# Optimization experiments

Measured on AMD Instinct MI355X. Metric: run time of the kernel, lower is better.

Reference implementation:

```python
import jax, jax.numpy as jnp
import numpy as np

# ---- static configuration (matches init_kwargs) ----
B = 32
H = 56
W = 56
C = 192
HEADS = 6
WS = 7            # window size
SHIFT = 3         # shift size (WS // 2)
MLP_HIDDEN = 768  # 4 * C
CPB = 256         # clip(56*56//16, 256, 1024)
N = WS * WS       # tokens per window
NW = (H // WS) * (W // WS)  # windows per image
EPS = 1e-5

# ---- static tables (Swin V2 continuous relative position bias) ----
# log-spaced relative coords table: [(2*WS-1)^2, 2]
_r = np.arange(-(WS - 1), WS, dtype=np.float32)
_tab = np.stack(np.meshgrid(_r, _r, indexing='ij'), axis=-1)  # [2WS-1, 2WS-1, 2]
_tab = _tab / (WS - 1) * 8.0  # pretrained_window_size=0 -> use window_size-1
_tab = np.sign(_tab) * np.log2(np.abs(_tab) + 1.0) / np.log2(8.0)
REL_TABLE = jnp.asarray(_tab.reshape(-1, 2))

# relative position index: [N, N] into the (2WS-1)^2 table
_coords = np.stack(np.meshgrid(np.arange(WS), np.arange(WS), indexing='ij'))
_cf = _coords.reshape(2, -1)
_rel = (_cf[:, :, None] - _cf[:, None, :]).transpose(1, 2, 0).astype(np.int64)
_rel[..., 0] += WS - 1
_rel[..., 1] += WS - 1
_rel[..., 0] *= 2 * WS - 1
REL_INDEX = jnp.asarray(_rel.sum(-1))

# shifted-window attention mask: [NW, N, N] with 0 / -100
_img = np.zeros((H, W), dtype=np.float32)
_sl = [slice(0, -WS), slice(-WS, -SHIFT), slice(-SHIFT, None)]
_cnt = 0
for _hs in _sl:
    for _ws in _sl:
        _img[_hs, _ws] = _cnt
        _cnt += 1
_mw = _img.reshape(H // WS, WS, W // WS, WS).transpose(0, 2, 1, 3).reshape(-1, N)
_am = _mw[:, None, :] - _mw[:, :, None]
ATTN_MASK = jnp.asarray(np.where(_am != 0, -100.0, 0.0).astype(np.float32))


def _layer_norm(x, g, b):
    mu = jnp.mean(x, axis=-1, keepdims=True)
    var = jnp.mean(jnp.square(x - mu), axis=-1, keepdims=True)
    return (x - mu) * jax.lax.rsqrt(var + EPS) * g + b


def setup_inputs() -> dict:
    key = jax.random.key(0)
    ks = jax.random.split(key, 10)
    def n(k, shape, s=0.02):
        return jax.random.normal(k, shape, jnp.float32) * s
    return {
        'x': jax.random.normal(ks[0], (B, H * W, C), jnp.float32),
        'qkv_w': n(ks[1], (3 * C, C)),
        'q_bias': jnp.zeros((C,), jnp.float32),
        'v_bias': jnp.zeros((C,), jnp.float32),
        'logit_scale': jnp.full((HEADS, 1, 1), jnp.log(10.0), jnp.float32),
        'cpb_w1': n(ks[2], (CPB, 2)),
        'cpb_b1': jnp.zeros((CPB,), jnp.float32),
        'cpb_w2': n(ks[3], (HEADS, CPB)),
        'proj_w': n(ks[4], (C, C)),
        'proj_b': jnp.zeros((C,), jnp.float32),
        'norm1_g': jnp.ones((C,), jnp.float32),
        'norm1_b': jnp.zeros((C,), jnp.float32),
        'norm2_g': jnp.ones((C,), jnp.float32),
        'norm2_b': jnp.zeros((C,), jnp.float32),
        'fc1_w': n(ks[5], (MLP_HIDDEN, C)),
        'fc1_b': jnp.zeros((MLP_HIDDEN,), jnp.float32),
        'fc2_w': n(ks[6], (C, MLP_HIDDEN)),
        'fc2_b': jnp.zeros((C,), jnp.float32),
    }


def reference(x, qkv_w, q_bias, v_bias, logit_scale, cpb_w1, cpb_b1, cpb_w2,
              proj_w, proj_b, norm1_g, norm1_b, norm2_g, norm2_b,
              fc1_w, fc1_b, fc2_w, fc2_b):
    b = x.shape[0]
    hd = C // HEADS
    shortcut = x

    # cyclic shift + window partition -> [b*NW, N, C]
    xi = jnp.roll(x.reshape(b, H, W, C), (-SHIFT, -SHIFT), axis=(1, 2))
    xw = xi.reshape(b, H // WS, WS, W // WS, WS, C)
    xw = xw.transpose(0, 1, 3, 2, 4, 5).reshape(-1, N, C)

    # qkv projection (k has no bias, per Swin V2)
    qkv_bias = jnp.concatenate([q_bias, jnp.zeros_like(q_bias), v_bias])
    qkv = (xw @ qkv_w.T + qkv_bias).reshape(-1, N, 3, HEADS, hd)
    qkv = qkv.transpose(2, 0, 3, 1, 4)  # [3, bw, heads, N, hd]
    q, k, v = qkv[0], qkv[1], qkv[2]

    # cosine attention with learned logit scale
    q = q / jnp.maximum(jnp.linalg.norm(q, axis=-1, keepdims=True), 1e-12)
    k = k / jnp.maximum(jnp.linalg.norm(k, axis=-1, keepdims=True), 1e-12)
    scale = jnp.exp(jnp.minimum(logit_scale, jnp.log(100.0)))  # [heads,1,1]
    attn = jnp.einsum('bhnd,bhmd->bhnm', q, k) * scale

    # continuous relative position bias via tiny MLP
    tab = jax.nn.relu(REL_TABLE @ cpb_w1.T + cpb_b1) @ cpb_w2.T  # [(2WS-1)^2, heads]
    rpb = 16.0 * jax.nn.sigmoid(tab[REL_INDEX])                  # [N, N, heads]
    attn = attn + rpb.transpose(2, 0, 1)[None]

    # shifted-window mask + softmax
    attn = attn.reshape(-1, NW, HEADS, N, N) + ATTN_MASK[None, :, None]
    attn = jax.nn.softmax(attn.reshape(-1, HEADS, N, N), axis=-1)

    out = jnp.einsum('bhnm,bhmd->bhnd', attn, v)
    out = out.transpose(0, 2, 1, 3).reshape(-1, N, C) @ proj_w.T + proj_b

    # window reverse + reverse shift
    xr = out.reshape(b, H // WS, W // WS, WS, WS, C)
    xr = xr.transpose(0, 1, 3, 2, 4, 5).reshape(b, H, W, C)
    xr = jnp.roll(xr, (SHIFT, SHIFT), axis=(1, 2)).reshape(b, H * W, C)

    # post-norm residual (Swin V2 style)
    x1 = shortcut + _layer_norm(xr, norm1_g, norm1_b)
    hmid = jax.nn.silu(x1 @ fc1_w.T + fc1_b) @ fc2_w.T + fc2_b
    return x1 + _layer_norm(hmid, norm2_g, norm2_b)
```

## Files before the change

kernel.cpp:

```cpp
#include <hip/hip_runtime.h>


typedef unsigned short ushort_t;
using f32x4  = __attribute__((ext_vector_type(4))) float;
using short8 = __attribute__((ext_vector_type(8))) short;
union LD16 { short8 v; ushort4 h[2]; };

__device__ __forceinline__ ushort_t f2bf(float f) {
  union { float f; unsigned u; } v; v.f = f;
  unsigned r = v.u + 0x7fffu + ((v.u >> 16) & 1u);
  return (ushort_t)(r >> 16);
}
__device__ __forceinline__ float bf2f(ushort_t u) {
  union { unsigned u; float f; } v; v.u = ((unsigned)u) << 16;
  return v.f;
}

__device__ __forceinline__ int img_pos(int m) {
  int win = m / 49, n = m - win * 49;
  int b = win >> 6, wi = win & 63;
  int nd = n / 7, nm = n - nd * 7;
  int hs = (wi >> 3) * 7 + nd;
  int ws = (wi & 7) * 7 + nm;
  int h = hs + 3; if (h >= 56) h -= 56;
  int w = ws + 3; if (w >= 56) w -= 56;
  return b * 3136 + h * 56 + w;
}

__device__ __forceinline__ int region3(int a) { return a < 49 ? 0 : (a < 53 ? 1 : 2); }

__global__ void cvt_kernel(const float* __restrict__ in, ushort_t* __restrict__ out, int n) {
  int i = blockIdx.x * 256 + threadIdx.x;
  if (i < n) out[i] = f2bf(in[i]);
}

__global__ __launch_bounds__(256) void gather_cvt_kernel(
    const float* __restrict__ x, ushort_t* __restrict__ xw) {
  int i8 = blockIdx.x * 256 + threadIdx.x;
  int m = i8 / 24, c8 = (i8 - m * 24) * 8;
  const float* p = x + (size_t)img_pos(m) * 192 + c8;
  float4 a = *(const float4*)p, b = *(const float4*)(p + 4);
  ushort_t* q = xw + (size_t)m * 192 + c8;
  *(ushort4*)q       = make_ushort4(f2bf(a.x), f2bf(a.y), f2bf(a.z), f2bf(a.w));
  *(ushort4*)(q + 4) = make_ushort4(f2bf(b.x), f2bf(b.y), f2bf(b.z), f2bf(b.w));
}

__global__ __launch_bounds__(256) void cpb_kernel(
    const float* __restrict__ w1, const float* __restrict__ b1,
    const float* __restrict__ w2, float* __restrict__ tab_s) {
  int e = blockIdx.x;
  int t = threadIdx.x;
  int i = e / 13, j = e - 13 * (e / 13);
  auto cval = [](int a) -> float {
    float r = (a - 6) * (8.0f / 6.0f);
    float v = log2f(fabsf(r) + 1.f) * (1.f / 3.f);
    return r < 0.f ? -v : v;
  };
  float ci = cval(i), cj = cval(j);
  float h = fmaxf(ci * w1[2 * t] + cj * w1[2 * t + 1] + b1[t], 0.f);
  __shared__ float red[256];
  for (int head = 0; head < 6; ++head) {
    red[t] = h * w2[head * 256 + t];
    __syncthreads();
    for (int st = 128; st > 0; st >>= 1) {
      if (t < st) red[t] += red[t + st];
      __syncthreads();
    }
    if (t == 0) tab_s[head * 169 + e] = 16.f / (1.f + __expf(-red[0]));
    __syncthreads();
  }
}

template<int NCHUNK, int MODE>
__global__ __launch_bounds__(512, 4) void gemm_persistA(
    const ushort_t* __restrict__ Ab, const ushort_t* __restrict__ W,
    const float* __restrict__ b0, const float* __restrict__ b1,
    ushort_t* __restrict__ out, int NTOT) {
  __shared__ ushort_t Al[128][200];
  __shared__ ushort_t Bl[192][40];
  int t = threadIdx.x;
  int m0 = blockIdx.x * 128;
  int lane = t & 63, wid = t >> 6;
  int wm = wid >> 1, wn = wid & 1;
  int lr = lane & 15, lg = lane >> 4;

#pragma unroll
  for (int s = 0; s < 6; ++s) {
    int task = t + (s << 9);
    int row = task / 24, j = task - row * 24;
    int blk = (j >> 2) << 5, jj = j & 3;
    int b4 = ((jj & 1) << 4) | ((jj >> 1) << 2);
    LD16 v; v.v = *(const short8*)(Ab + (size_t)(m0 + row) * 192 + j * 8);
    *(ushort4*)&Al[row][blk + b4]     = v.h[0];
    *(ushort4*)&Al[row][blk + b4 + 8] = v.h[1];
  }

  bool stager = (t < 256);
  int bn = (t & 255) >> 2, cB = t & 3;
  int colB = ((cB & 1) << 4) | ((cB >> 1) << 2);

  for (int c = 0; c < NCHUNK; ++c) {
    int n0 = c * 192;
    const ushort_t* Browp  = W + (size_t)(n0 + bn) * 192 + (cB << 3);
    const ushort_t* Browp2 = W + (size_t)(n0 + 64 + bn) * 192 + (cB << 3);
    const ushort_t* Browp3 = W + (size_t)(n0 + 128 + bn) * 192 + (cB << 3);
    LD16 B0, B1, B2;
    auto LOADB = [&](int kt) {
      B0.v = *(const short8*)(Browp + kt);
      B1.v = *(const short8*)(Browp2 + kt);
      B2.v = *(const short8*)(Browp3 + kt);
    };

    f32x4 acc[2][6];
#pragma unroll
    for (int a = 0; a < 2; ++a)
#pragma unroll
      for (int b = 0; b < 6; ++b) acc[a][b] = (f32x4){0.f, 0.f, 0.f, 0.f};

    if (stager) LOADB(0);
    for (int it = 0; it < 6; ++it) {
      if (stager) {
        ushort_t* Br0 = &Bl[bn][0];
        *(ushort4*)(Br0 + colB + 0) = B0.h[0];
        *(ushort4*)(Br0 + colB + 8) = B0.h[1];
        ushort_t* Br1 = &Bl[64 + bn][0];
        *(ushort4*)(Br1 + colB + 0) = B1.h[0];
        *(ushort4*)(Br1 + colB + 8) = B1.h[1];
        ushort_t* Br2 = &Bl[128 + bn][0];
        *(ushort4*)(Br2 + colB + 0) = B2.h[0];
        *(ushort4*)(Br2 + colB + 8) = B2.h[1];
      }
      __syncthreads();
      if (stager && it + 1 < 6) LOADB((it + 1) * 32);
      short8 af[2], bfv[6];
#pragma unroll
      for (int fm = 0; fm < 2; ++fm)
        af[fm] = *(const short8*)&Al[wm * 32 + fm * 16 + lr][it * 32 + lg * 8];
#pragma unroll
      for (int fn = 0; fn < 6; ++fn)
        bfv[fn] = *(const short8*)&Bl[wn * 96 + fn * 16 + lr][lg * 8];
#pragma unroll
      for (int fm = 0; fm < 2; ++fm)
#pragma unroll
        for (int fn = 0; fn < 6; ++fn)
          acc[fm][fn] = __builtin_amdgcn_mfma_f32_16x16x32_bf16(af[fm], bfv[fn], acc[fm][fn], 0, 0, 0);
      __syncthreads();
    }

#pragma unroll
    for (int fm = 0; fm < 2; ++fm) {
#pragma unroll
      for (int fn = 0; fn < 6; ++fn) {
        int col = n0 + wn * 96 + fn * 16 + lr;
        float bias;
        if (MODE == 0) bias = (col < 192) ? b0[col] : ((col < 384) ? 0.f : b1[col - 384]);
        else           bias = b0[col];
#pragma unroll
        for (int r = 0; r < 4; ++r) {
          int row = m0 + wm * 32 + fm * 16 + lg * 4 + r;
          float v = acc[fm][fn][r] + bias;
          if (MODE == 1) v = v / (1.f + __expf(-v));
          out[(size_t)row * NTOT + col] = f2bf(v);
        }
      }
    }
  }
}

__global__ __launch_bounds__(512, 4) void gemm_fc2(
    const ushort_t* __restrict__ Ab, const ushort_t* __restrict__ W,
    const float* __restrict__ b0, float* __restrict__ outf) {
  const int KTOT = 768, NTOT = 192;
  __shared__ ushort_t Al[128][40];
  __shared__ ushort_t Bl[192][40];
  int t = threadIdx.x;
  int m0 = blockIdx.x * 128;
  int lane = t & 63, wid = t >> 6;
  int wm = wid >> 1, wn = wid & 1;
  int lr = lane & 15, lg = lane >> 4;

  bool stager = (t < 256);
  int arow = (t & 255) >> 1, akoff = (t & 1) << 4;
  const ushort_t* Arowp = Ab + (size_t)(m0 + arow) * KTOT + akoff;
  int colA = akoff ? 4 : 0;
  int bn = (t & 255) >> 2, cB = t & 3;
  const ushort_t* Browp  = W + (size_t)(bn) * KTOT + (cB << 3);
  const ushort_t* Browp2 = W + (size_t)(64 + bn) * KTOT + (cB << 3);
  const ushort_t* Browp3 = W + (size_t)(128 + bn) * KTOT + (cB << 3);
  int colB = ((cB & 1) << 4) | ((cB >> 1) << 2);

  f32x4 acc[2][6];
#pragma unroll
  for (int a = 0; a < 2; ++a)
#pragma unroll
    for (int b = 0; b < 6; ++b) acc[a][b] = (f32x4){0.f, 0.f, 0.f, 0.f};

  LD16 A01, A23, B0, B1, B2;
  auto LOADREGS = [&](int kt) {
    A01.v = *(const short8*)(Arowp + kt);
    A23.v = *(const short8*)(Arowp + kt + 8);
    B0.v  = *(const short8*)(Browp + kt);
    B1.v  = *(const short8*)(Browp2 + kt);
    B2.v  = *(const short8*)(Browp3 + kt);
  };

  const int NT = KTOT / 32;
  if (stager) LOADREGS(0);
  for (int it = 0; it < NT; ++it) {
    if (stager) {
      ushort_t* Ar = &Al[arow][0];
      *(ushort4*)(Ar + colA +  0) = A01.h[0];
      *(ushort4*)(Ar + colA +  8) = A01.h[1];
      *(ushort4*)(Ar + colA + 16) = A23.h[0];
      *(ushort4*)(Ar + colA + 24) = A23.h[1];
      ushort_t* Br0 = &Bl[bn][0];
      *(ushort4*)(Br0 + colB + 0) = B0.h[0];
      *(ushort4*)(Br0 + colB + 8) = B0.h[1];
      ushort_t* Br1 = &Bl[64 + bn][0];
      *(ushort4*)(Br1 + colB + 0) = B1.h[0];
      *(ushort4*)(Br1 + colB + 8) = B1.h[1];
      ushort_t* Br2 = &Bl[128 + bn][0];
      *(ushort4*)(Br2 + colB + 0) = B2.h[0];
      *(ushort4*)(Br2 + colB + 8) = B2.h[1];
    }
    __syncthreads();
    if (stager && it + 1 < NT) LOADREGS((it + 1) * 32);
    short8 af[2], bfv[6];
#pragma unroll
    for (int fm = 0; fm < 2; ++fm)
      af[fm] = *(const short8*)&Al[wm * 32 + fm * 16 + lr][lg * 8];
#pragma unroll
    for (int fn = 0; fn < 6; ++fn)
      bfv[fn] = *(const short8*)&Bl[wn * 96 + fn * 16 + lr][lg * 8];
#pragma unroll
    for (int fm = 0; fm < 2; ++fm)
#pragma unroll
      for (int fn = 0; fn < 6; ++fn)
        acc[fm][fn] = __builtin_amdgcn_mfma_f32_16x16x32_bf16(af[fm], bfv[fn], acc[fm][fn], 0, 0, 0);
    if (it + 1 < NT) __syncthreads();
  }
#pragma unroll
  for (int fm = 0; fm < 2; ++fm) {
#pragma unroll
    for (int fn = 0; fn < 6; ++fn) {
      int col = wn * 96 + fn * 16 + lr;
      float bias = b0[col];
#pragma unroll
      for (int r = 0; r < 4; ++r) {
        int row = m0 + wm * 32 + fm * 16 + lg * 4 + r;
        outf[(size_t)row * NTOT + col] = acc[fm][fn][r] + bias;
      }
    }
  }
}

template<int MODE>
__global__ __launch_bounds__(256) void ln_resid_kernel(
    const ushort_t* __restrict__ pre, const float* __restrict__ residf,
    const ushort_t* __restrict__ residb, const float* __restrict__ gamma,
    const float* __restrict__ beta, ushort_t* __restrict__ outb,
    float* outio) {
  int m = (blockIdx.x * 256 + threadIdx.x) >> 6;
  int lane = threadIdx.x & 63;
  float v0, v1, v2;
  if (MODE == 0) {
    const ushort_t* p = pre + (size_t)m * 192;
    v0 = bf2f(p[lane]); v1 = bf2f(p[lane + 64]); v2 = bf2f(p[lane + 128]);
  } else {
    const float* p = outio + (size_t)m * 192;
    v0 = p[lane]; v1 = p[lane + 64]; v2 = p[lane + 128];
  }
  float s1 = v0 + v1 + v2;
  float s2 = v0 * v0 + v1 * v1 + v2 * v2;
#pragma unroll
  for (int o = 1; o < 64; o <<= 1) {
    s1 += __shfl_xor(s1, o);
    s2 += __shfl_xor(s2, o);
  }
  float mean = s1 * (1.f / 192.f);
  float var  = s2 * (1.f / 192.f) - mean * mean;
  float rstd = rsqrtf(fmaxf(var, 0.f) + 1e-5f);
  float l0 = (v0 - mean) * rstd * gamma[lane]       + beta[lane];
  float l1 = (v1 - mean) * rstd * gamma[lane + 64]  + beta[lane + 64];
  float l2 = (v2 - mean) * rstd * gamma[lane + 128] + beta[lane + 128];
  if (MODE == 0) {
    size_t og = (size_t)img_pos(m) * 192;
    outb[og + lane]       = f2bf(residf[og + lane]       + l0);
    outb[og + lane + 64]  = f2bf(residf[og + lane + 64]  + l1);
    outb[og + lane + 128] = f2bf(residf[og + lane + 128] + l2);
  } else {
    size_t og = (size_t)m * 192;
    outio[og + lane]       = bf2f(residb[og + lane])       + l0;
    outio[og + lane + 64]  = bf2f(residb[og + lane + 64])  + l1;
    outio[og + lane + 128] = bf2f(residb[og + lane + 128]) + l2;
  }
}

__global__ __launch_bounds__(256) void attn_kernel(
    const ushort_t* __restrict__ qkv, const float* __restrict__ logit_scale,
    const float* __restrict__ tab_s, ushort_t* __restrict__ attn_out) {
  __shared__ ushort_t qs[64][40];
  __shared__ ushort_t ksl[64][40];
  __shared__ ushort_t vsl[32][80];
  __shared__ ushort_t ps[64][80];
  __shared__ float tab_l[169];
  int win = blockIdx.x, head = blockIdx.y;
  int t = threadIdx.x;
  int wi = win & 63;
  int wh0 = (wi >> 3) * 7, ww0 = (wi & 7) * 7;
  size_t base = (size_t)win * 49 * 576 + head * 32;

  for (int u = t; u < 169; u += 256) tab_l[u] = tab_s[head * 169 + u];

  for (int u = t; u < 240; u += 256) {
    int arr = u / 120, v = u - arr * 120;
    int r = 49 + (v >> 3), c4 = (v & 7) << 2;
    ushort_t* p = arr ? &ksl[r][c4] : &qs[r][c4];
    *(ushort4*)p = make_ushort4(0, 0, 0, 0);
  }

  for (int u = t; u < 2048; u += 256) {
    int key = u >> 5, d = u & 31;
    ushort_t val = 0;
    if (key < 49) val = qkv[base + (size_t)key * 576 + 384 + d];
    int kk = key & 31;
    int pc = ((key >> 5) << 5) + 8 * ((kk >> 2) & 3) + 4 * (kk >> 4) + (kk & 3);
    vsl[d][pc] = val;
  }

  float scale = __expf(fminf(logit_scale[head], 4.605170186f));

  if (t < 196) {
    int r = t >> 2, c = t & 3;
    const ushort_t* qp = qkv + base + (size_t)r * 576 + c * 8;
    ushort4 qa = *(const ushort4*)qp,         qb = *(const ushort4*)(qp + 4);
    ushort4 ka = *(const ushort4*)(qp + 192), kb = *(const ushort4*)(qp + 196);
    float qf[8] = {bf2f(qa.x), bf2f(qa.y), bf2f(qa.z), bf2f(qa.w),
                   bf2f(qb.x), bf2f(qb.y), bf2f(qb.z), bf2f(qb.w)};
    float kf[8] = {bf2f(ka.x), bf2f(ka.y), bf2f(ka.z), bf2f(ka.w),
                   bf2f(kb.x), bf2f(kb.y), bf2f(kb.z), bf2f(kb.w)};
    float sq = 0.f, sk = 0.f;
#pragma unroll
    for (int d = 0; d < 8; ++d) { sq += qf[d] * qf[d]; sk += kf[d] * kf[d]; }
    sq += __shfl_xor(sq, 1); sq += __shfl_xor(sq, 2);
    sk += __shfl_xor(sk, 1); sk += __shfl_xor(sk, 2);
    float rq = scale / fmaxf(sqrtf(sq), 1e-12f);
    float rk = 1.f   / fmaxf(sqrtf(sk), 1e-12f);
    int c0 = ((c & 1) << 4) | ((c >> 1) << 2);
    ushort_t* qd = &qs[r][c0];
    *(ushort4*)(qd + 0) = make_ushort4(f2bf(qf[0]*rq), f2bf(qf[1]*rq), f2bf(qf[2]*rq), f2bf(qf[3]*rq));
    *(ushort4*)(qd + 8) = make_ushort4(f2bf(qf[4]*rq), f2bf(qf[5]*rq), f2bf(qf[6]*rq), f2bf(qf[7]*rq));
    ushort_t* kd = &ksl[r][c0];
    *(ushort4*)(kd + 0) = make_ushort4(f2bf(kf[0]*rk), f2bf(kf[1]*rk), f2bf(kf[2]*rk), f2bf(kf[3]*rk));
    *(ushort4*)(kd + 8) = make_ushort4(f2bf(kf[4]*rk), f2bf(kf[5]*rk), f2bf(kf[6]*rk), f2bf(kf[7]*rk));
  }
  __syncthreads();

  int lane = t & 63, w = t >> 6;
  int lr = lane & 15, lg = lane >> 4;

  short8 aq = *(const short8*)&qs[w * 16 + lr][lg * 8];
  f32x4 acc[4];
#pragma unroll
  for (int fn = 0; fn < 4; ++fn) {
    acc[fn] = (f32x4){0.f, 0.f, 0.f, 0.f};
    short8 bk = *(const short8*)&ksl[fn * 16 + lr][lg * 8];
    acc[fn] = __builtin_amdgcn_mfma_f32_16x16x32_bf16(aq, bk, acc[fn], 0, 0, 0);
  }

  float rsum[4];
#pragma unroll
  for (int r = 0; r < 4; ++r) {
    int row = w * 16 + lg * 4 + r;
    int rd = (row * 9363) >> 16, rm = row - 7 * rd;
    int gr = region3(wh0 + rd) * 3 + region3(ww0 + rm);
    bool rv = row < 49;
    float sv[4];
#pragma unroll
    for (int fn = 0; fn < 4; ++fn) {
      int col = fn * 16 + lr;
      int jd = (col * 9363) >> 16, jm = col - 7 * jd;
      int gj = region3(wh0 + jd) * 3 + region3(ww0 + jm);
      bool cv = rv && (col < 49);
      int idx = cv ? (rd - jd + 6) * 13 + (rm - jm + 6) : 0;
      float s = acc[fn][r] + tab_l[idx] + (gr == gj ? 0.f : -100.f);
      sv[fn] = cv ? s : -1e30f;
    }
    float m = fmaxf(fmaxf(sv[0], sv[1]), fmaxf(sv[2], sv[3]));
#pragma unroll
    for (int o = 1; o < 16; o <<= 1) m = fmaxf(m, __shfl_xor(m, o));
    float sum = 0.f;
#pragma unroll
    for (int fn = 0; fn < 4; ++fn) {
      float e = __expf(sv[fn] - m);
      sum += e;
      int pc = ((fn >> 1) << 5) + 8 * (lr >> 2) + ((fn & 1) << 2) + (lr & 3);
      ps[row][pc] = f2bf(e);
    }
#pragma unroll
    for (int o = 1; o < 16; o <<= 1) sum += __shfl_xor(sum, o);
    rsum[r] = 1.f / sum;
  }
  __syncthreads();

  short8 ap0 = *(const short8*)&ps[w * 16 + lr][lg * 8];
  short8 ap1 = *(const short8*)&ps[w * 16 + lr][32 + lg * 8];
  f32x4 o2[2];
#pragma unroll
  for (int f = 0; f < 2; ++f) {
    o2[f] = (f32x4){0.f, 0.f, 0.f, 0.f};
    short8 bv0 = *(const short8*)&vsl[f * 16 + lr][lg * 8];
    short8 bv1 = *(const short8*)&vsl[f * 16 + lr][32 + lg * 8];
    o2[f] = __builtin_amdgcn_mfma_f32_16x16x32_bf16(ap0, bv0, o2[f], 0, 0, 0);
    o2[f] = __builtin_amdgcn_mfma_f32_16x16x32_bf16(ap1, bv1, o2[f], 0, 0, 0);
  }
#pragma unroll
  for (int f = 0; f < 2; ++f) {
#pragma unroll
    for (int r = 0; r < 4; ++r) {
      int row = w * 16 + lg * 4 + r;
      if (row < 49)
        attn_out[((size_t)win * 49 + row) * 192 + head * 32 + f * 16 + lr] =
            f2bf(o2[f][r] * rsum[r]);
    }
  }
}

extern "C" void kernel_launch(void* const* d_in, const int* in_sizes, int n_in,
                              void* d_out, int out_size, void* d_ws, size_t ws_size,
                              hipStream_t stream) {
  (void)in_sizes; (void)n_in; (void)out_size; (void)ws_size;
  const float* x    = (const float*)d_in[0];
  const float* qkvw = (const float*)d_in[1];
  const float* qb   = (const float*)d_in[2];
  const float* vb   = (const float*)d_in[3];
  const float* ls   = (const float*)d_in[4];
  const float* cw1  = (const float*)d_in[5];
  const float* cb1  = (const float*)d_in[6];
  const float* cw2  = (const float*)d_in[7];
  const float* pw   = (const float*)d_in[8];
  const float* pb   = (const float*)d_in[9];
  const float* n1g  = (const float*)d_in[10];
  const float* n1b  = (const float*)d_in[11];
  const float* n2g  = (const float*)d_in[12];
  const float* n2b  = (const float*)d_in[13];
  const float* f1w  = (const float*)d_in[14];
  const float* f1b  = (const float*)d_in[15];
  const float* f2w  = (const float*)d_in[16];
  const float* f2b  = (const float*)d_in[17];
  float* out = (float*)d_out;

  char* ws = (char*)d_ws;
  ushort_t* wq_bf = (ushort_t*)ws;
  ushort_t* wp_bf = wq_bf + 110592;
  ushort_t* w1_bf = wp_bf + 36864;
  ushort_t* w2_bf = w1_bf + 147456;
  float*    tab_s = (float*)(w2_bf + 147456);
  const size_t OFF_BIG = 1 << 20;
  ushort_t* qkv_out = (ushort_t*)(ws + OFF_BIG);
  ushort_t* xw_bf   = (ushort_t*)(ws + OFF_BIG + 115605504);
  ushort_t* attn_o  = (ushort_t*)(ws + OFF_BIG + 115605504);
  ushort_t* x1_bf   = (ushort_t*)(ws + OFF_BIG + 154140672);
  ushort_t* hmid    = (ushort_t*)(ws + OFF_BIG);

  cvt_kernel<<<(110592 + 255) / 256, 256, 0, stream>>>(qkvw, wq_bf, 110592);
  cvt_kernel<<<(36864  + 255) / 256, 256, 0, stream>>>(pw,   wp_bf, 36864);
  cvt_kernel<<<(147456 + 255) / 256, 256, 0, stream>>>(f1w,  w1_bf, 147456);
  cvt_kernel<<<(147456 + 255) / 256, 256, 0, stream>>>(f2w,  w2_bf, 147456);
  cpb_kernel<<<169, 256, 0, stream>>>(cw1, cb1, cw2, tab_s);
  gather_cvt_kernel<<<9408, 256, 0, stream>>>(x, xw_bf);

  gemm_persistA<3, 0><<<784, 512, 0, stream>>>(xw_bf, wq_bf, qb, vb, qkv_out, 576);
  attn_kernel<<<dim3(2048, 6), 256, 0, stream>>>(qkv_out, ls, tab_s, attn_o);
  gemm_persistA<1, 2><<<784, 512, 0, stream>>>(attn_o, wp_bf, pb, nullptr, attn_o, 192);
  ln_resid_kernel<0><<<25088, 256, 0, stream>>>(attn_o, x, nullptr, n1g, n1b, x1_bf, nullptr);
  gemm_persistA<4, 1><<<784, 512, 0, stream>>>(x1_bf, w1_bf, f1b, nullptr, hmid, 768);
  gemm_fc2<<<784, 512, 0, stream>>>(hmid, w2_bf, f2b, out);
  ln_resid_kernel<1><<<25088, 256, 0, stream>>>(nullptr, nullptr, x1_bf, n2g, n2b, nullptr, out);
}
```

Before: 400.4 us.

## Fuse LayerNorm-residual epilogues into proj/fc2 GEMMs and split N across grid

Adds a GEMM kernel that computes the full 192-wide output row tile and then performs the post-norm LayerNorm plus residual add in the epilogue. Row statistics are reduced across the two N-warps through shared memory. This removes the two standalone ln_resid passes and their intermediate reads and writes. It also replaces the persistent-A QKV and fc1 GEMMs with a 2D grid (blockIdx.y over 192-column chunks) that streams A in K-tiles, raising block count but reloading A per chunk. The proj GEMM no longer writes its intermediate in place over attn_o.

```diff
diff --git a/kernel.cpp b/kernel.cpp
--- a/kernel.cpp
+++ b/kernel.cpp
@@ -71,110 +71,15 @@
   }
 }
 
-template<int NCHUNK, int MODE>
-__global__ __launch_bounds__(512, 4) void gemm_persistA(
+template<int KTOT, int MODE>
+__global__ __launch_bounds__(512, 4) void gemm_n192(
     const ushort_t* __restrict__ Ab, const ushort_t* __restrict__ W,
     const float* __restrict__ b0, const float* __restrict__ b1,
     ushort_t* __restrict__ out, int NTOT) {
-  __shared__ ushort_t Al[128][200];
-  __shared__ ushort_t Bl[192][40];
-  int t = threadIdx.x;
-  int m0 = blockIdx.x * 128;
-  int lane = t & 63, wid = t >> 6;
-  int wm = wid >> 1, wn = wid & 1;
-  int lr = lane & 15, lg = lane >> 4;
-
-#pragma unroll
-  for (int s = 0; s < 6; ++s) {
-    int task = t + (s << 9);
-    int row = task / 24, j = task - row * 24;
-    int blk = (j >> 2) << 5, jj = j & 3;
-    int b4 = ((jj & 1) << 4) | ((jj >> 1) << 2);
-    LD16 v; v.v = *(const short8*)(Ab + (size_t)(m0 + row) * 192 + j * 8);
-    *(ushort4*)&Al[row][blk + b4]     = v.h[0];
-    *(ushort4*)&Al[row][blk + b4 + 8] = v.h[1];
-  }
-
-  bool stager = (t < 256);
-  int bn = (t & 255) >> 2, cB = t & 3;
-  int colB = ((cB & 1) << 4) | ((cB >> 1) << 2);
-
-  for (int c = 0; c < NCHUNK; ++c) {
-    int n0 = c * 192;
-    const ushort_t* Browp  = W + (size_t)(n0 + bn) * 192 + (cB << 3);
-    const ushort_t* Browp2 = W + (size_t)(n0 + 64 + bn) * 192 + (cB << 3);
-    const ushort_t* Browp3 = W + (size_t)(n0 + 128 + bn) * 192 + (cB << 3);
-    LD16 B0, B1, B2;
-    auto LOADB = [&](int kt) {
-      B0.v = *(const short8*)(Browp + kt);
-      B1.v = *(const short8*)(Browp2 + kt);
-      B2.v = *(const short8*)(Browp3 + kt);
-    };
-
-    f32x4 acc[2][6];
-#pragma unroll
-    for (int a = 0; a < 2; ++a)
-#pragma unroll
-      for (int b = 0; b < 6; ++b) acc[a][b] = (f32x4){0.f, 0.f, 0.f, 0.f};
-
-    if (stager) LOADB(0);
-    for (int it = 0; it < 6; ++it) {
-      if (stager) {
-        ushort_t* Br0 = &Bl[bn][0];
-        *(ushort4*)(Br0 + colB + 0) = B0.h[0];
-        *(ushort4*)(Br0 + colB + 8) = B0.h[1];
-        ushort_t* Br1 = &Bl[64 + bn][0];
-        *(ushort4*)(Br1 + colB + 0) = B1.h[0];
-        *(ushort4*)(Br1 + colB + 8) = B1.h[1];
-        ushort_t* Br2 = &Bl[128 + bn][0];
-        *(ushort4*)(Br2 + colB + 0) = B2.h[0];
-        *(ushort4*)(Br2 + colB + 8) = B2.h[1];
-      }
-      __syncthreads();
-      if (stager && it + 1 < 6) LOADB((it + 1) * 32);
-      short8 af[2], bfv[6];
-#pragma unroll
-      for (int fm = 0; fm < 2; ++fm)
-        af[fm] = *(const short8*)&Al[wm * 32 + fm * 16 + lr][it * 32 + lg * 8];
-#pragma unroll
-      for (int fn = 0; fn < 6; ++fn)
-        bfv[fn] = *(const short8*)&Bl[wn * 96 + fn * 16 + lr][lg * 8];
-#pragma unroll
-      for (int fm = 0; fm < 2; ++fm)
-#pragma unroll
-        for (int fn = 0; fn < 6; ++fn)
-          acc[fm][fn] = __builtin_amdgcn_mfma_f32_16x16x32_bf16(af[fm], bfv[fn], acc[fm][fn], 0, 0, 0);
-      __syncthreads();
-    }
-
-#pragma unroll
-    for (int fm = 0; fm < 2; ++fm) {
-#pragma unroll
-      for (int fn = 0; fn < 6; ++fn) {
-        int col = n0 + wn * 96 + fn * 16 + lr;
-        float bias;
-        if (MODE == 0) bias = (col < 192) ? b0[col] : ((col < 384) ? 0.f : b1[col - 384]);
-        else           bias = b0[col];
-#pragma unroll
-        for (int r = 0; r < 4; ++r) {
-          int row = m0 + wm * 32 + fm * 16 + lg * 4 + r;
-          float v = acc[fm][fn][r] + bias;
-          if (MODE == 1) v = v / (1.f + __expf(-v));
-          out[(size_t)row * NTOT + col] = f2bf(v);
-        }
-      }
-    }
-  }
-}
-
-__global__ __launch_bounds__(512, 4) void gemm_fc2(
-    const ushort_t* __restrict__ Ab, const ushort_t* __restrict__ W,
-    const float* __restrict__ b0, float* __restrict__ outf) {
-  const int KTOT = 768, NTOT = 192;
   __shared__ ushort_t Al[128][40];
   __shared__ ushort_t Bl[192][40];
   int t = threadIdx.x;
-  int m0 = blockIdx.x * 128;
+  int m0 = blockIdx.x * 128, n0 = blockIdx.y * 192;
   int lane = t & 63, wid = t >> 6;
   int wm = wid >> 1, wn = wid & 1;
   int lr = lane & 15, lg = lane >> 4;
@@ -184,9 +89,9 @@
   const ushort_t* Arowp = Ab + (size_t)(m0 + arow) * KTOT + akoff;
   int colA = akoff ? 4 : 0;
   int bn = (t & 255) >> 2, cB = t & 3;
-  const ushort_t* Browp  = W + (size_t)(bn) * KTOT + (cB << 3);
-  const ushort_t* Browp2 = W + (size_t)(64 + bn) * KTOT + (cB << 3);
-  const ushort_t* Browp3 = W + (size_t)(128 + bn) * KTOT + (cB << 3);
+  const ushort_t* Browp  = W + (size_t)(n0 + bn) * KTOT + (cB << 3);
+  const ushort_t* Browp2 = W + (size_t)(n0 + 64 + bn) * KTOT + (cB << 3);
+  const ushort_t* Browp3 = W + (size_t)(n0 + 128 + bn) * KTOT + (cB << 3);
   int colB = ((cB & 1) << 4) | ((cB >> 1) << 2);
 
   f32x4 acc[2][6];
@@ -243,56 +148,143 @@
   for (int fm = 0; fm < 2; ++fm) {
 #pragma unroll
     for (int fn = 0; fn < 6; ++fn) {
-      int col = wn * 96 + fn * 16 + lr;
-      float bias = b0[col];
+      int col = n0 + wn * 96 + fn * 16 + lr;
+      float bias;
+      if (MODE == 0) bias = (col < 192) ? b0[col] : ((col < 384) ? 0.f : b1[col - 384]);
+      else           bias = b0[col];
 #pragma unroll
       for (int r = 0; r < 4; ++r) {
         int row = m0 + wm * 32 + fm * 16 + lg * 4 + r;
-        outf[(size_t)row * NTOT + col] = acc[fm][fn][r] + bias;
+        float v = acc[fm][fn][r] + bias;
+        if (MODE == 1) v = v / (1.f + __expf(-v));
+        out[(size_t)row * NTOT + col] = f2bf(v);
       }
     }
   }
 }
 
-template<int MODE>
-__global__ __launch_bounds__(256) void ln_resid_kernel(
-    const ushort_t* __restrict__ pre, const float* __restrict__ residf,
-    const ushort_t* __restrict__ residb, const float* __restrict__ gamma,
-    const float* __restrict__ beta, ushort_t* __restrict__ outb,
-    float* outio) {
-  int m = (blockIdx.x * 256 + threadIdx.x) >> 6;
-  int lane = threadIdx.x & 63;
-  float v0, v1, v2;
-  if (MODE == 0) {
-    const ushort_t* p = pre + (size_t)m * 192;
-    v0 = bf2f(p[lane]); v1 = bf2f(p[lane + 64]); v2 = bf2f(p[lane + 128]);
-  } else {
-    const float* p = outio + (size_t)m * 192;
-    v0 = p[lane]; v1 = p[lane + 64]; v2 = p[lane + 128];
-  }
-  float s1 = v0 + v1 + v2;
-  float s2 = v0 * v0 + v1 * v1 + v2 * v2;
-#pragma unroll
-  for (int o = 1; o < 64; o <<= 1) {
-    s1 += __shfl_xor(s1, o);
-    s2 += __shfl_xor(s2, o);
-  }
-  float mean = s1 * (1.f / 192.f);
-  float var  = s2 * (1.f / 192.f) - mean * mean;
-  float rstd = rsqrtf(fmaxf(var, 0.f) + 1e-5f);
-  float l0 = (v0 - mean) * rstd * gamma[lane]       + beta[lane];
-  float l1 = (v1 - mean) * rstd * gamma[lane + 64]  + beta[lane + 64];
-  float l2 = (v2 - mean) * rstd * gamma[lane + 128] + beta[lane + 128];
-  if (MODE == 0) {
-    size_t og = (size_t)img_pos(m) * 192;
-    outb[og + lane]       = f2bf(residf[og + lane]       + l0);
-    outb[og + lane + 64]  = f2bf(residf[og + lane + 64]  + l1);
-    outb[og + lane + 128] = f2bf(residf[og + lane + 128] + l2);
-  } else {
-    size_t og = (size_t)m * 192;
-    outio[og + lane]       = bf2f(residb[og + lane])       + l0;
-    outio[og + lane + 64]  = bf2f(residb[og + lane + 64])  + l1;
-    outio[og + lane + 128] = bf2f(residb[og + lane + 128]) + l2;
+template<int KTOT, int MODE>
+__global__ __launch_bounds__(512, 4) void gemm_ln512(
+    const ushort_t* __restrict__ Ab, const ushort_t* __restrict__ W,
+    const float* __restrict__ bias, const float* __restrict__ gamma,
+    const float* __restrict__ beta, const float* __restrict__ residf,
+    const ushort_t* __restrict__ residb, ushort_t* __restrict__ outb,
+    float* __restrict__ outf) {
+  __shared__ ushort_t Al[128][40];
+  __shared__ ushort_t Bl[192][40];
+  int t = threadIdx.x;
+  int m0 = blockIdx.x * 128;
+  int lane = t & 63, wid = t >> 6;
+  int wm = wid >> 1, wn = wid & 1;
+  int lr = lane & 15, lg = lane >> 4;
+
+  bool stager = (t < 256);
+  int arow = (t & 255) >> 1, akoff = (t & 1) << 4;
+  const ushort_t* Arowp = Ab + (size_t)(m0 + arow) * KTOT + akoff;
+  int colA = akoff ? 4 : 0;
+  int bn = (t & 255) >> 2, cB = t & 3;
+  const ushort_t* Browp  = W + (size_t)(bn) * KTOT + (cB << 3);
+  const ushort_t* Browp2 = W + (size_t)(64 + bn) * KTOT + (cB << 3);
+  const ushort_t* Browp3 = W + (size_t)(128 + bn) * KTOT + (cB << 3);
+  int colB = ((cB & 1) << 4) | ((cB >> 1) << 2);
+
+  f32x4 acc[2][6];
+#pragma unroll
+  for (int a = 0; a < 2; ++a)
+#pragma unroll
+    for (int b = 0; b < 6; ++b) acc[a][b] = (f32x4){0.f, 0.f, 0.f, 0.f};
+
+  LD16 A01, A23, B0, B1, B2;
+  auto LOADREGS = [&](int kt) {
+    A01.v = *(const short8*)(Arowp + kt);
+    A23.v = *(const short8*)(Arowp + kt + 8);
+    B0.v  = *(const short8*)(Browp + kt);
+    B1.v  = *(const short8*)(Browp2 + kt);
+    B2.v  = *(const short8*)(Browp3 + kt);
+  };
+
+  const int NT = KTOT / 32;
+  if (stager) LOADREGS(0);
+  for (int it = 0; it < NT; ++it) {
+    if (stager) {
+      ushort_t* Ar = &Al[arow][0];
+      *(ushort4*)(Ar + colA +  0) = A01.h[0];
+      *(ushort4*)(Ar + colA +  8) = A01.h[1];
+      *(ushort4*)(Ar + colA + 16) = A23.h[0];
+      *(ushort4*)(Ar + colA + 24) = A23.h[1];
+      ushort_t* Br0 = &Bl[bn][0];
+      *(ushort4*)(Br0 + colB + 0) = B0.h[0];
+      *(ushort4*)(Br0 + colB + 8) = B0.h[1];
+      ushort_t* Br1 = &Bl[64 + bn][0];
+      *(ushort4*)(Br1 + colB + 0) = B1.h[0];
+      *(ushort4*)(Br1 + colB + 8) = B1.h[1];
+      ushort_t* Br2 = &Bl[128 + bn][0];
+      *(ushort4*)(Br2 + colB + 0) = B2.h[0];
+      *(ushort4*)(Br2 + colB + 8) = B2.h[1];
+    }
+    __syncthreads();
+    if (stager && it + 1 < NT) LOADREGS((it + 1) * 32);
+    short8 af[2], bfv[6];
+#pragma unroll
+    for (int fm = 0; fm < 2; ++fm)
+      af[fm] = *(const short8*)&Al[wm * 32 + fm * 16 + lr][lg * 8];
+#pragma unroll
+    for (int fn = 0; fn < 6; ++fn)
+      bfv[fn] = *(const short8*)&Bl[wn * 96 + fn * 16 + lr][lg * 8];
+#pragma unroll
+    for (int fm = 0; fm < 2; ++fm)
+#pragma unroll
+      for (int fn = 0; fn < 6; ++fn)
+        acc[fm][fn] = __builtin_amdgcn_mfma_f32_16x16x32_bf16(af[fm], bfv[fn], acc[fm][fn], 0, 0, 0);
+    __syncthreads();
+  }
+
+  float* part = (float*)&Bl[0][0];
+#pragma unroll
+  for (int fm = 0; fm < 2; ++fm) {
+#pragma unroll
+    for (int r = 0; r < 4; ++r) {
+      float s1 = 0.f, s2 = 0.f;
+#pragma unroll
+      for (int fn = 0; fn < 6; ++fn) {
+        int col = wn * 96 + fn * 16 + lr;
+        float v = acc[fm][fn][r] + bias[col];
+        acc[fm][fn][r] = v;
+        s1 += v; s2 += v * v;
+      }
+#pragma unroll
+      for (int off = 1; off < 16; off <<= 1) {
+        s1 += __shfl_xor(s1, off);
+        s2 += __shfl_xor(s2, off);
+      }
+      if (lr == 0) {
+        int lrow = wm * 32 + fm * 16 + lg * 4 + r;
+        part[(wn * 128 + lrow) * 2 + 0] = s1;
+        part[(wn * 128 + lrow) * 2 + 1] = s2;
+      }
+    }
+  }
+  __syncthreads();
+#pragma unroll
+  for (int fm = 0; fm < 2; ++fm) {
+#pragma unroll
+    for (int r = 0; r < 4; ++r) {
+      int lrow = wm * 32 + fm * 16 + lg * 4 + r;
+      float s1 = part[lrow * 2 + 0] + part[(128 + lrow) * 2 + 0];
+      float s2 = part[lrow * 2 + 1] + part[(128 + lrow) * 2 + 1];
+      float mean = s1 * (1.f / 192.f);
+      float var  = s2 * (1.f / 192.f) - mean * mean;
+      float rstd = rsqrtf(fmaxf(var, 0.f) + 1e-5f);
+      int rg = m0 + lrow;
+      size_t og = (MODE == 0 ? (size_t)img_pos(rg) : (size_t)rg) * 192;
+#pragma unroll
+      for (int fn = 0; fn < 6; ++fn) {
+        int col = wn * 96 + fn * 16 + lr;
+        float l = (acc[fm][fn][r] - mean) * rstd * gamma[col] + beta[col];
+        if (MODE == 0) outb[og + col] = f2bf(residf[og + col] + l);
+        else           outf[og + col] = bf2f(residb[og + col]) + l;
+      }
+    }
   }
 }
 
@@ -470,11 +462,9 @@
   cpb_kernel<<<169, 256, 0, stream>>>(cw1, cb1, cw2, tab_s);
   gather_cvt_kernel<<<9408, 256, 0, stream>>>(x, xw_bf);
 
-  gemm_persistA<3, 0><<<784, 512, 0, stream>>>(xw_bf, wq_bf, qb, vb, qkv_out, 576);
+  gemm_n192<192, 0><<<dim3(784, 3), 512, 0, stream>>>(xw_bf, wq_bf, qb, vb, qkv_out, 576);
   attn_kernel<<<dim3(2048, 6), 256, 0, stream>>>(qkv_out, ls, tab_s, attn_o);
-  gemm_persistA<1, 2><<<784, 512, 0, stream>>>(attn_o, wp_bf, pb, nullptr, attn_o, 192);
-  ln_resid_kernel<0><<<25088, 256, 0, stream>>>(attn_o, x, nullptr, n1g, n1b, x1_bf, nullptr);
-  gemm_persistA<4, 1><<<784, 512, 0, stream>>>(x1_bf, w1_bf, f1b, nullptr, hmid, 768);
-  gemm_fc2<<<784, 512, 0, stream>>>(hmid, w2_bf, f2b, out);
-  ln_resid_kernel<1><<<25088, 256, 0, stream>>>(nullptr, nullptr, x1_bf, n2g, n2b, nullptr, out);
-}
+  gemm_ln512<192, 0><<<784, 512, 0, stream>>>(attn_o, wp_bf, pb, n1g, n1b, x, nullptr, x1_bf, nullptr);
+  gemm_n192<192, 1><<<dim3(784, 4), 512, 0, stream>>>(x1_bf, w1_bf, f1b, nullptr, hmid, 768);
+  gemm_ln512<768, 1><<<784, 512, 0, stream>>>(hmid, w2_bf, f2b, n2g, n2b, nullptr, x1_bf, nullptr, out);
+}
```

Measured after the change: 413.1 us. +3.2%, slower.
